# Optimization experiments

Measured on AMD Instinct MI355X. Metric: run time of the kernel, lower is better.

## Reference

```python
import jax, jax.numpy as jnp
import numpy as np

D_MODEL = 1024
N_HEADS = 16
D_K = D_MODEL // N_HEADS
B, S = 4, 2048


def setup_inputs() -> dict:
    key = jax.random.key(0)
    ks = jax.random.split(key, 5)
    scale = 1.0 / np.sqrt(D_MODEL)  # ~xavier scale for square matrices
    return {
        "Q": jax.random.normal(ks[0], (B, S, D_MODEL), dtype=jnp.float32),
        "length": jax.random.randint(ks[1], (B,), 1, S, dtype=jnp.int32),
        "Wq": jax.random.normal(ks[2], (D_MODEL, D_MODEL), dtype=jnp.float32) * scale,
        "bq": jnp.zeros((D_MODEL,), dtype=jnp.float32),
        "Wk": jax.random.normal(ks[3], (D_MODEL, D_MODEL), dtype=jnp.float32) * scale,
        "bk": jnp.zeros((D_MODEL,), dtype=jnp.float32),
        "Wv": jax.random.normal(ks[4], (D_MODEL, D_MODEL), dtype=jnp.float32) * scale,
        "bv": jnp.zeros((D_MODEL,), dtype=jnp.float32),
    }


def reference(Q, length, Wq, bq, Wk, bk, Wv, bv):
    b, s, d = Q.shape
    q_a = Q @ Wq + bq                                   # [b, s, d]
    # split heads: [b, h, s, d_k]
    q_s = q_a.reshape(b, s, N_HEADS, D_K).transpose(0, 2, 1, 3)
    k_s = (Q @ Wk + bk).reshape(b, s, N_HEADS, D_K).transpose(0, 2, 1, 3)
    v_s = (Q @ Wv + bv).reshape(b, s, N_HEADS, D_K).transpose(0, 2, 1, 3)

    # unnormalized exp attention with multiplicative key mask (faithful to source)
    scores = jnp.einsum("bhqd,bhkd->bhqk", q_s, k_s) / np.sqrt(D_K)
    scores = jnp.exp(scores)
    key_mask = (jnp.arange(s)[None, :] < length[:, None]).astype(scores.dtype)  # [b, k]
    scores = scores * key_mask[:, None, None, :]        # broadcast over heads, queries
    attn = scores / (jnp.sum(scores, axis=-1, keepdims=True) + 1e-8)
    context = jnp.einsum("bhqk,bhkd->bhqd", attn, v_s)
    context = context.transpose(0, 2, 1, 3).reshape(b, s, d)
    return context, q_a
```

## Files before the change

kernel.cpp:

```cpp
#include <hip/hip_runtime.h>

#define D_MODEL 1024
#define N_HEADS 16
#define D_KH    64
#define BATCH   4
#define SEQ     2048
#define M_TOTAL (BATCH*SEQ)

typedef __attribute__((ext_vector_type(8))) short short8;
typedef __attribute__((ext_vector_type(4))) float f32x4;
typedef __attribute__((ext_vector_type(4))) unsigned short u16x4;
typedef __attribute__((ext_vector_type(2))) unsigned int u32x2;

__device__ __forceinline__ unsigned short f2bf(float f) {
  union { float f; unsigned u; } v; v.f = f;
  unsigned r = v.u + 0x7FFFu + ((v.u >> 16) & 1u);
  return (unsigned short)(r >> 16);
}
__device__ __forceinline__ unsigned fbits(float f) {
  union { float f; unsigned u; } v; v.f = f; return v.u;
}

__global__ __launch_bounds__(256) void cvt_all(
    const float* __restrict__ Q, unsigned short* __restrict__ Qbf,
    const float* __restrict__ Wq, const float* __restrict__ Wk,
    const float* __restrict__ Wv, unsigned short* __restrict__ WT) {
  __shared__ float tile[32][33];
  const int bid = blockIdx.x;
  if (bid < 8192) {
    size_t i = (size_t)bid * 256 + threadIdx.x;
    float4 v = ((const float4*)Q)[i];
    u16x4 o;
    o[0] = f2bf(v.x); o[1] = f2bf(v.y); o[2] = f2bf(v.z); o[3] = f2bf(v.w);
    ((u16x4*)Qbf)[i] = o;
  } else {
    const int r = bid - 8192;
    const int z = r >> 10;
    const int rem = r & 1023;
    const int k0 = (rem >> 5) * 32, n0 = (rem & 31) * 32;
    const float* W = (z == 0) ? Wq : (z == 1) ? Wk : Wv;
    const int tx = threadIdx.x & 31, ty = threadIdx.x >> 5;
    for (int i = 0; i < 4; ++i)
      tile[ty + i * 8][tx] = W[(size_t)(k0 + ty + i * 8) * D_MODEL + n0 + tx];
    __syncthreads();
    unsigned short* out = WT + (size_t)z * D_MODEL * D_MODEL;
    for (int i = 0; i < 4; ++i)
      out[(size_t)(n0 + ty + i * 8) * D_MODEL + k0 + tx] = f2bf(tile[tx][ty + i * 8]);
  }
}

#define GQ_BM 128
#define GQ_BN 128
#define GQ_BK 64
#define GQ_NT (D_MODEL / GQ_BK)

__global__ __launch_bounds__(256, 2) void gemm_qkv(
    const unsigned short* __restrict__ Qbf,
    const unsigned short* __restrict__ WT,
    const float* __restrict__ bq_p, const float* __restrict__ bk_p,
    const float* __restrict__ bv_p,
    float* __restrict__ out_qa,
    unsigned short* __restrict__ kbf,
    unsigned short* __restrict__ vt) {
  const int f   = blockIdx.x;
  const int swz = (f & 7) * 192 + (f >> 3);
  const int mm  = swz / 24;
  const int nn  = swz % 24;
  const int m0  = mm * GQ_BM;
  const int n0g = nn * GQ_BN;
  const int z   = n0g >> 10;
  const int n0  = n0g & 1023;

  __shared__ unsigned short smA[2][GQ_BM * GQ_BK];
  __shared__ unsigned short smB[2][GQ_BN * GQ_BK];

  const int t    = threadIdx.x;
  const int lane = t & 63;
  const int w    = t >> 6;
  const int quad = lane >> 4;
  const int l16  = lane & 15;
  const int wr   = w >> 1, wc = w & 1;

  f32x4 acc[4][4];
  for (int i = 0; i < 4; ++i)
    for (int j = 0; j < 4; ++j) acc[i][j] = (f32x4){0.f, 0.f, 0.f, 0.f};

  auto stage = [&](int p, int kt) {
    #pragma unroll
    for (int r = 0; r < 4; ++r) {
      int o   = (r * 256 + t) * 8;
      int row = o >> 6;
      int col = (o & 63) ^ ((row & 7) << 3);
      const unsigned short* ga = Qbf + (size_t)(m0 + row)  * D_MODEL + kt * 64 + col;
      const unsigned short* gb = WT  + (size_t)(n0g + row) * D_MODEL + kt * 64 + col;
      __builtin_amdgcn_global_load_lds(
          (const __attribute__((address_space(1))) void*)ga,
          (__attribute__((address_space(3))) void*)&smA[p][o], 16, 0, 0);
      __builtin_amdgcn_global_load_lds(
          (const __attribute__((address_space(1))) void*)gb,
          (__attribute__((address_space(3))) void*)&smB[p][o], 16, 0, 0);
    }
  };

  stage(0, 0);
  stage(1, 1);
  asm volatile("s_waitcnt vmcnt(8)" ::: "memory");
  __builtin_amdgcn_s_barrier();
  asm volatile("" ::: "memory");

  for (int kt = 0; kt < GQ_NT; ++kt) {
    const int p = kt & 1;

    short8 af[4][2], bf[4][2];
    #pragma unroll
    for (int mi = 0; mi < 4; ++mi) {
      int row = wr * 64 + mi * 16 + l16;
      #pragma unroll
      for (int kk = 0; kk < 2; ++kk)
        af[mi][kk] = *(const short8*)
            &smA[p][(row * 64 + kk * 32 + quad * 8) ^ ((row & 7) << 3)];
    }
    #pragma unroll
    for (int ni = 0; ni < 4; ++ni) {
      int row = wc * 64 + ni * 16 + l16;
      #pragma unroll
      for (int kk = 0; kk < 2; ++kk)
        bf[ni][kk] = *(const short8*)
            &smB[p][(row * 64 + kk * 32 + quad * 8) ^ ((row & 7) << 3)];
    }

    __builtin_amdgcn_s_setprio(1);
    #pragma unroll
    for (int mi = 0; mi < 4; ++mi)
      #pragma unroll
      for (int ni = 0; ni < 4; ++ni) {
        acc[mi][ni] = __builtin_amdgcn_mfma_f32_16x16x32_bf16(
            af[mi][0], bf[ni][0], acc[mi][ni], 0, 0, 0);
        acc[mi][ni] = __builtin_amdgcn_mfma_f32_16x16x32_bf16(
            af[mi][1], bf[ni][1], acc[mi][ni], 0, 0, 0);
      }
    __builtin_amdgcn_s_setprio(0);

    __builtin_amdgcn_s_barrier();
    asm volatile("" ::: "memory");
    if (kt + 2 < GQ_NT) {
      stage(p, kt + 2);
      asm volatile("s_waitcnt vmcnt(8)" ::: "memory");
    } else {
      asm volatile("s_waitcnt vmcnt(0)" ::: "memory");
    }
    __builtin_amdgcn_s_barrier();
    asm volatile("" ::: "memory");
  }

  const float* bias = (z == 0) ? bq_p : (z == 1) ? bk_p : bv_p;
  if (z == 2) {
    for (int ni = 0; ni < 4; ++ni) {
      int n = n0 + wc * 64 + ni * 16 + l16;
      float bval = bias[n];
      int h = n >> 6, d = n & 63;
      for (int mi = 0; mi < 4; ++mi) {
        int m = m0 + wr * 64 + mi * 16 + quad * 4;
        int b = m >> 11, s = m & 2047;
        u16x4 o;
        for (int j = 0; j < 4; ++j) o[j] = f2bf(acc[mi][ni][j] + bval);
        *(u16x4*)&vt[(size_t)((b * 16 + h) * 64 + d) * SEQ + s] = o;
      }
    }
  } else {
    for (int ni = 0; ni < 4; ++ni) {
      int n = n0 + wc * 64 + ni * 16 + l16;
      float bval = bias[n];
      for (int mi = 0; mi < 4; ++mi) {
        int mbase = m0 + wr * 64 + mi * 16 + quad * 4;
        for (int j = 0; j < 4; ++j) {
          float v = acc[mi][ni][j] + bval;
          size_t idx = (size_t)(mbase + j) * D_MODEL + n;
          if (z == 0) out_qa[idx] = v;
          else        kbf[idx] = f2bf(v);
        }
      }
    }
  }
}

#define PST 72
#define QBLK 128

__global__ __launch_bounds__(256, 4) void attn(
    const float* __restrict__ qa,
    const unsigned short* __restrict__ kbf,
    const unsigned short* __restrict__ vt,
    const int* __restrict__ length,
    float* __restrict__ ctx) {
  const int flat = blockIdx.y * 16 + blockIdx.x;
  const int low = flat & 3;
  const int mid = (flat >> 2) & 15;
  const int hi  = flat >> 6;
  const int b  = (low + mid + (mid >> 2) + hi + (hi >> 2)) & 3;
  const int h  = mid;
  const int qt = hi;
  const int bh = b * 16 + h;
  const int len = length[b];

  const int t    = threadIdx.x;
  const int lane = t & 63;
  const int w    = t >> 6;
  const int quad = lane >> 4;
  const int l16  = lane & 15;
  const int r8   = t >> 3;
  const int c8   = (t & 7) * 8;

  __shared__ unsigned short sQ[QBLK * PST];
  __shared__ unsigned short sK[64 * PST];
  __shared__ unsigned short sVT[64 * PST];
  unsigned short* const sP = sQ;

  const float SCL = 0.125f * 1.44269504f;

  for (int half = 0; half < 4; ++half) {
    int r = r8 + half * 32;
    const float* src = qa + (size_t)(b * SEQ + qt * QBLK + r) * D_MODEL + h * D_KH + c8;
    float4 v0 = *(const float4*)src;
    float4 v1 = *(const float4*)(src + 4);
    short8 o;
    o[0] = (short)f2bf(v0.x * SCL); o[1] = (short)f2bf(v0.y * SCL);
    o[2] = (short)f2bf(v0.z * SCL); o[3] = (short)f2bf(v0.w * SCL);
    o[4] = (short)f2bf(v1.x * SCL); o[5] = (short)f2bf(v1.y * SCL);
    o[6] = (short)f2bf(v1.z * SCL); o[7] = (short)f2bf(v1.w * SCL);
    *(short8*)&sQ[r * PST + c8] = o;
  }
  __syncthreads();

  const int qr0 = w * 16 + l16;
  const int qr1 = 64 + qr0;
  short8 qf00 = *(const short8*)&sQ[qr0 * PST + quad * 8];
  short8 qf01 = *(const short8*)&sQ[qr0 * PST + 32 + quad * 8];
  short8 qf10 = *(const short8*)&sQ[qr1 * PST + quad * 8];
  short8 qf11 = *(const short8*)&sQ[qr1 * PST + 32 + quad * 8];

  f32x4 acc0[4], acc1[4];
  for (int i = 0; i < 4; ++i) {
    acc0[i] = (f32x4){0.f, 0.f, 0.f, 0.f};
    acc1[i] = (f32x4){0.f, 0.f, 0.f, 0.f};
  }
  float den0 = 0.f, den1 = 0.f;

  const unsigned short* kbase_p = kbf + (size_t)b * SEQ * D_MODEL + h * D_KH;
  const unsigned short* vbase_p = vt + (size_t)bh * 64 * SEQ;

  const int nkt = (len + 63) >> 6;

  short8 rk[2], rv[2];
  for (int half = 0; half < 2; ++half) {
    int r = r8 + half * 32;
    rk[half] = *(const short8*)(kbase_p + (size_t)r * D_MODEL + c8);
    rv[half] = *(const short8*)(vbase_p + (size_t)r * SEQ + c8);
  }

  for (int kt = 0; kt < nkt; ++kt) {
    __syncthreads();
    for (int half = 0; half < 2; ++half) {
      int r = r8 + half * 32;
      *(short8*)&sK[r * PST + c8]  = rk[half];
      *(short8*)&sVT[r * PST + c8] = rv[half];
    }
    __syncthreads();

    if (kt + 1 < nkt) {
      for (int half = 0; half < 2; ++half) {
        int r = r8 + half * 32;
        rk[half] = *(const short8*)(kbase_p + (size_t)((kt + 1) * 64 + r) * D_MODEL + c8);
        rv[half] = *(const short8*)(vbase_p + (size_t)r * SEQ + (kt + 1) * 64 + c8);
      }
    }

    const bool full = ((kt + 1) << 6) <= len;

    for (int n = 0; n < 4; ++n) {
      short8 kf0 = *(const short8*)&sK[(n * 16 + l16) * PST + quad * 8];
      short8 kf1 = *(const short8*)&sK[(n * 16 + l16) * PST + 32 + quad * 8];
      f32x4 s0 = (f32x4){0.f, 0.f, 0.f, 0.f};
      s0 = __builtin_amdgcn_mfma_f32_16x16x32_bf16(kf0, qf00, s0, 0, 0, 0);
      s0 = __builtin_amdgcn_mfma_f32_16x16x32_bf16(kf1, qf01, s0, 0, 0, 0);
      f32x4 s1 = (f32x4){0.f, 0.f, 0.f, 0.f};
      s1 = __builtin_amdgcn_mfma_f32_16x16x32_bf16(kf0, qf10, s1, 0, 0, 0);
      s1 = __builtin_amdgcn_mfma_f32_16x16x32_bf16(kf1, qf11, s1, 0, 0, 0);

      float e0, e1, e2, e3, f0, f1, f2, f3;
      if (full) {
        e0 = exp2f(s0[0]); e1 = exp2f(s0[1]); e2 = exp2f(s0[2]); e3 = exp2f(s0[3]);
        f0 = exp2f(s1[0]); f1 = exp2f(s1[1]); f2 = exp2f(s1[2]); f3 = exp2f(s1[3]);
      } else {
        int kb = kt * 64 + n * 16 + quad * 4;
        e0 = (kb + 0 < len) ? exp2f(s0[0]) : 0.f;
        e1 = (kb + 1 < len) ? exp2f(s0[1]) : 0.f;
        e2 = (kb + 2 < len) ? exp2f(s0[2]) : 0.f;
        e3 = (kb + 3 < len) ? exp2f(s0[3]) : 0.f;
        f0 = (kb + 0 < len) ? exp2f(s1[0]) : 0.f;
        f1 = (kb + 1 < len) ? exp2f(s1[1]) : 0.f;
        f2 = (kb + 2 < len) ? exp2f(s1[2]) : 0.f;
        f3 = (kb + 3 < len) ? exp2f(s1[3]) : 0.f;
      }
      den0 += (e0 + e1) + (e2 + e3);
      den1 += (f0 + f1) + (f2 + f3);
      u32x2 pk;
      pk[0] = __builtin_amdgcn_perm(fbits(e1), fbits(e0), 0x07060302);
      pk[1] = __builtin_amdgcn_perm(fbits(e3), fbits(e2), 0x07060302);
      *(u32x2*)&sP[qr0 * PST + n * 16 + quad * 4] = pk;
      u32x2 pk1;
      pk1[0] = __builtin_amdgcn_perm(fbits(f1), fbits(f0), 0x07060302);
      pk1[1] = __builtin_amdgcn_perm(fbits(f3), fbits(f2), 0x07060302);
      *(u32x2*)&sP[qr1 * PST + n * 16 + quad * 4] = pk1;
    }

    short8 pf00 = *(const short8*)&sP[qr0 * PST + quad * 8];
    short8 pf01 = *(const short8*)&sP[qr0 * PST + 32 + quad * 8];
    short8 pf10 = *(const short8*)&sP[qr1 * PST + quad * 8];
    short8 pf11 = *(const short8*)&sP[qr1 * PST + 32 + quad * 8];
    for (int n2 = 0; n2 < 4; ++n2) {
      short8 vf0 = *(const short8*)&sVT[(n2 * 16 + l16) * PST + quad * 8];
      short8 vf1 = *(const short8*)&sVT[(n2 * 16 + l16) * PST + 32 + quad * 8];
      acc0[n2] = __builtin_amdgcn_mfma_f32_16x16x32_bf16(vf0, pf00, acc0[n2], 0, 0, 0);
      acc0[n2] = __builtin_amdgcn_mfma_f32_16x16x32_bf16(vf1, pf01, acc0[n2], 0, 0, 0);
      acc1[n2] = __builtin_amdgcn_mfma_f32_16x16x32_bf16(vf0, pf10, acc1[n2], 0, 0, 0);
      acc1[n2] = __builtin_amdgcn_mfma_f32_16x16x32_bf16(vf1, pf11, acc1[n2], 0, 0, 0);
    }
  }

  den0 += __shfl_xor(den0, 16, 64);
  den0 += __shfl_xor(den0, 32, 64);
  den1 += __shfl_xor(den1, 16, 64);
  den1 += __shfl_xor(den1, 32, 64);
  float inv0 = 1.f / (den0 + 1e-8f);
  float inv1 = 1.f / (den1 + 1e-8f);

  {
    int q0 = qt * QBLK + w * 16 + l16;
    float* dst0 = ctx + (size_t)(b * SEQ + q0) * D_MODEL + h * D_KH;
    float* dst1 = dst0 + (size_t)64 * D_MODEL;
    for (int n2 = 0; n2 < 4; ++n2) {
      f32x4 o0 = acc0[n2];
      f32x4 o1 = acc1[n2];
      *(float4*)(dst0 + n2 * 16 + quad * 4) =
          make_float4(o0[0] * inv0, o0[1] * inv0, o0[2] * inv0, o0[3] * inv0);
      *(float4*)(dst1 + n2 * 16 + quad * 4) =
          make_float4(o1[0] * inv1, o1[1] * inv1, o1[2] * inv1, o1[3] * inv1);
    }
  }
}

extern "C" void kernel_launch(void* const* d_in, const int* in_sizes, int n_in,
                              void* d_out, int out_size, void* d_ws, size_t ws_size,
                              hipStream_t stream) {
  const float* Q      = (const float*)d_in[0];
  const int*   length = (const int*)d_in[1];
  const float* Wq     = (const float*)d_in[2];
  const float* bq     = (const float*)d_in[3];
  const float* Wk     = (const float*)d_in[4];
  const float* bk     = (const float*)d_in[5];
  const float* Wv     = (const float*)d_in[6];
  const float* bv     = (const float*)d_in[7];

  float* out_ctx = (float*)d_out;
  float* out_qa  = out_ctx + (size_t)M_TOTAL * D_MODEL;

  char* ws = (char*)d_ws;
  unsigned short* Qbf = (unsigned short*)ws;
  unsigned short* WT  = (unsigned short*)(ws + (size_t)16 * 1024 * 1024);
  unsigned short* Kbf = (unsigned short*)(ws + (size_t)22 * 1024 * 1024);
  unsigned short* Vt  = (unsigned short*)(ws + (size_t)38 * 1024 * 1024);

  hipLaunchKernelGGL(cvt_all, dim3(8192 + 3072), dim3(256), 0, stream,
                     Q, Qbf, Wq, Wk, Wv, WT);
  hipLaunchKernelGGL(gemm_qkv, dim3(64 * 24), dim3(256), 0, stream,
                     Qbf, WT, bq, bk, bv, out_qa, Kbf, Vt);
  hipLaunchKernelGGL(attn, dim3(SEQ / QBLK, BATCH * N_HEADS), dim3(256), 0, stream,
                     out_qa, Kbf, Vt, length, out_ctx);
}
```

Before: 241.4 us.

## Restructure QKV GEMM into 256x256 tiles with 8-wave phased half-tile pipeline

The QKV projection GEMM moves from 128x128 tiles with 4 waves to 256x256 tiles with 8 waves (512 threads), cutting the grid from 1536 to 384 blocks. Each K-tile is split into A/B halves, and loads of the next half-tiles are interleaved with the MFMA work on the current quadrants in eight phases per two K-steps, each phase with its own fine-grained vmcnt wait and barriers. The aim is more data reuse per LDS byte and better overlap of global-to-LDS traffic with compute. The cost is 128 KB of LDS per block, higher register pressure from 32 accumulators, and a small grid of 384 blocks that may leave the 256 CUs poorly balanced.

```diff
diff --git a/kernel.cpp b/kernel.cpp
--- a/kernel.cpp
+++ b/kernel.cpp
@@ -19,6 +19,9 @@
 }
 __device__ __forceinline__ unsigned fbits(float f) {
   union { float f; unsigned u; } v; v.f = f; return v.u;
+}
+__device__ __forceinline__ int sw(int row, int col) {
+  return row * 64 + (col ^ ((row & 7) << 3));
 }
 
 __global__ __launch_bounds__(256) void cvt_all(
@@ -49,12 +52,66 @@
   }
 }
 
-#define GQ_BM 128
-#define GQ_BN 128
-#define GQ_BK 64
-#define GQ_NT (D_MODEL / GQ_BK)
-
-__global__ __launch_bounds__(256, 2) void gemm_qkv(
+#define GQ_NT 16
+
+#define GQ_STAGE_HALF(buf, tile, isB, half) do {                               \
+    int kt_ = (tile) & 15;                                                     \
+    _Pragma("unroll")                                                          \
+    for (int r_ = 0; r_ < 2; ++r_) {                                           \
+      int o_   = (r_ * 512 + t) * 8;                \
+      int row_ = (half) * 128 + (o_ >> 6);                                     \
+      int col_ = (o_ & 63) ^ ((row_ & 7) << 3);       \
+      const unsigned short* g_ = (isB)                                         \
+          ? WT  + (size_t)(n0g + row_) * D_MODEL + kt_ * 64 + col_             \
+          : Qbf + (size_t)(m0  + row_) * D_MODEL + kt_ * 64 + col_;            \
+      unsigned short* l_ = ((isB) ? &smB[buf][0] : &smA[buf][0])               \
+                           + (half) * 8192 + o_;              \
+      __builtin_amdgcn_global_load_lds(                                        \
+          (const __attribute__((address_space(1))) void*)g_,                   \
+          (__attribute__((address_space(3))) void*)l_, 16, 0, 0);              \
+    }                                                                          \
+  } while (0)
+
+#define GQ_PHASE(buf, ah, bh, WAIT4, stTile, stB, stHalf) do {                 \
+    short8 a_[2][4], b_[2][2];                                                 \
+    _Pragma("unroll")                                                          \
+    for (int kh_ = 0; kh_ < 2; ++kh_) {                                        \
+      _Pragma("unroll")                                                        \
+      for (int mi_ = 0; mi_ < 4; ++mi_) {                                      \
+        int row_ = (ah) * 128 + wr * 64 + mi_ * 16 + l16;                      \
+        a_[kh_][mi_] = *(const short8*)&smA[buf][sw(row_, kh_ * 32 + quad * 8)]; \
+      }                                                                        \
+      _Pragma("unroll")                                                        \
+      for (int ni_ = 0; ni_ < 2; ++ni_) {                                      \
+        int row_ = (bh) * 128 + wc * 32 + ni_ * 16 + l16;                      \
+        b_[kh_][ni_] = *(const short8*)&smB[buf][sw(row_, kh_ * 32 + quad * 8)]; \
+      }                                                                        \
+    }                                                                          \
+    GQ_STAGE_HALF(((stTile) & 1), stTile, stB, stHalf);                        \
+    __builtin_amdgcn_s_barrier();                                              \
+    asm volatile("" ::: "memory");                                             \
+    __builtin_amdgcn_s_setprio(1);                                             \
+    _Pragma("unroll")                                                          \
+    for (int mi_ = 0; mi_ < 4; ++mi_) {                                        \
+      _Pragma("unroll")                                                        \
+      for (int ni_ = 0; ni_ < 2; ++ni_) {                                      \
+        acc[(ah) * 4 + mi_][(bh) * 2 + ni_] =                                  \
+            __builtin_amdgcn_mfma_f32_16x16x32_bf16(                           \
+                a_[0][mi_], b_[0][ni_], acc[(ah) * 4 + mi_][(bh) * 2 + ni_],   \
+                0, 0, 0);                                                      \
+        acc[(ah) * 4 + mi_][(bh) * 2 + ni_] =                                  \
+            __builtin_amdgcn_mfma_f32_16x16x32_bf16(                           \
+                a_[1][mi_], b_[1][ni_], acc[(ah) * 4 + mi_][(bh) * 2 + ni_],   \
+                0, 0, 0);                                                      \
+      }                                                                        \
+    }                                                                          \
+    __builtin_amdgcn_s_setprio(0);                                             \
+    if (WAIT4) asm volatile("s_waitcnt vmcnt(4)" ::: "memory");                \
+    __builtin_amdgcn_s_barrier();                                              \
+    asm volatile("" ::: "memory");                                             \
+  } while (0)
+
+__global__ __launch_bounds__(512, 2) void gemm_qkv(
     const unsigned short* __restrict__ Qbf,
     const unsigned short* __restrict__ WT,
     const float* __restrict__ bq_p, const float* __restrict__ bk_p,
@@ -63,121 +120,99 @@
     unsigned short* __restrict__ kbf,
     unsigned short* __restrict__ vt) {
   const int f   = blockIdx.x;
-  const int swz = (f & 7) * 192 + (f >> 3);
-  const int mm  = swz / 24;
-  const int nn  = swz % 24;
-  const int m0  = mm * GQ_BM;
-  const int n0g = nn * GQ_BN;
+  const int swz = (f & 7) * 48 + (f >> 3);
+  const int mm  = swz / 12;
+  const int nn  = swz % 12;
+  const int m0  = mm * 256;
+  const int n0g = nn * 256;
   const int z   = n0g >> 10;
   const int n0  = n0g & 1023;
 
-  __shared__ unsigned short smA[2][GQ_BM * GQ_BK];
-  __shared__ unsigned short smB[2][GQ_BN * GQ_BK];
+  __shared__ unsigned short smA[2][256 * 64];
+  __shared__ unsigned short smB[2][256 * 64];
 
   const int t    = threadIdx.x;
   const int lane = t & 63;
   const int w    = t >> 6;
   const int quad = lane >> 4;
   const int l16  = lane & 15;
-  const int wr   = w >> 1, wc = w & 1;
-
-  f32x4 acc[4][4];
-  for (int i = 0; i < 4; ++i)
+  const int wr   = w >> 2;
+  const int wc   = w & 3;
+
+  f32x4 acc[8][4];
+  #pragma unroll
+  for (int i = 0; i < 8; ++i)
+    #pragma unroll
     for (int j = 0; j < 4; ++j) acc[i][j] = (f32x4){0.f, 0.f, 0.f, 0.f};
 
-  auto stage = [&](int p, int kt) {
-    #pragma unroll
-    for (int r = 0; r < 4; ++r) {
-      int o   = (r * 256 + t) * 8;
-      int row = o >> 6;
-      int col = (o & 63) ^ ((row & 7) << 3);
-      const unsigned short* ga = Qbf + (size_t)(m0 + row)  * D_MODEL + kt * 64 + col;
-      const unsigned short* gb = WT  + (size_t)(n0g + row) * D_MODEL + kt * 64 + col;
-      __builtin_amdgcn_global_load_lds(
-          (const __attribute__((address_space(1))) void*)ga,
-          (__attribute__((address_space(3))) void*)&smA[p][o], 16, 0, 0);
-      __builtin_amdgcn_global_load_lds(
-          (const __attribute__((address_space(1))) void*)gb,
-          (__attribute__((address_space(3))) void*)&smB[p][o], 16, 0, 0);
-    }
-  };
-
-  stage(0, 0);
-  stage(1, 1);
-  asm volatile("s_waitcnt vmcnt(8)" ::: "memory");
+  GQ_STAGE_HALF(0, 0, 0, 0);
+  GQ_STAGE_HALF(0, 0, 1, 1);
+  GQ_STAGE_HALF(0, 0, 1, 0);
+  GQ_STAGE_HALF(0, 0, 0, 1);
+  GQ_STAGE_HALF(1, 1, 0, 0);
+  GQ_STAGE_HALF(1, 1, 1, 1);
+  asm volatile("s_waitcnt vmcnt(4)" ::: "memory");
   __builtin_amdgcn_s_barrier();
   asm volatile("" ::: "memory");
 
-  for (int kt = 0; kt < GQ_NT; ++kt) {
-    const int p = kt & 1;
-
-    short8 af[4][2], bf[4][2];
-    #pragma unroll
-    for (int mi = 0; mi < 4; ++mi) {
-      int row = wr * 64 + mi * 16 + l16;
-      #pragma unroll
-      for (int kk = 0; kk < 2; ++kk)
-        af[mi][kk] = *(const short8*)
-            &smA[p][(row * 64 + kk * 32 + quad * 8) ^ ((row & 7) << 3)];
-    }
-    #pragma unroll
-    for (int ni = 0; ni < 4; ++ni) {
-      int row = wc * 64 + ni * 16 + l16;
-      #pragma unroll
-      for (int kk = 0; kk < 2; ++kk)
-        bf[ni][kk] = *(const short8*)
-            &smB[p][(row * 64 + kk * 32 + quad * 8) ^ ((row & 7) << 3)];
-    }
-
-    __builtin_amdgcn_s_setprio(1);
-    #pragma unroll
-    for (int mi = 0; mi < 4; ++mi)
-      #pragma unroll
-      for (int ni = 0; ni < 4; ++ni) {
-        acc[mi][ni] = __builtin_amdgcn_mfma_f32_16x16x32_bf16(
-            af[mi][0], bf[ni][0], acc[mi][ni], 0, 0, 0);
-        acc[mi][ni] = __builtin_amdgcn_mfma_f32_16x16x32_bf16(
-            af[mi][1], bf[ni][1], acc[mi][ni], 0, 0, 0);
-      }
-    __builtin_amdgcn_s_setprio(0);
-
-    __builtin_amdgcn_s_barrier();
-    asm volatile("" ::: "memory");
-    if (kt + 2 < GQ_NT) {
-      stage(p, kt + 2);
-      asm volatile("s_waitcnt vmcnt(8)" ::: "memory");
-    } else {
-      asm volatile("s_waitcnt vmcnt(0)" ::: "memory");
-    }
-    __builtin_amdgcn_s_barrier();
-    asm volatile("" ::: "memory");
-  }
+  for (int i = 0; i < GQ_NT / 2; ++i) {
+    const int e = 2 * i;
+    const int o = 2 * i + 1;
+    GQ_PHASE(0,  0, 0, 0,  o,        1,  0);
+    GQ_PHASE(0,  0, 1, 0,  o,        0,  1);
+    GQ_PHASE(0,  1, 1, 0,  e + 2,    0,  0);
+    GQ_PHASE(0,  1, 0, 1,  e + 2,    1,  1);
+    GQ_PHASE(1,  0, 0, 0,  e + 2,    1,  0);
+    GQ_PHASE(1,  0, 1, 0,  e + 2,    0,  1);
+    GQ_PHASE(1,  1, 1, 0,  o + 2,    0,  0);
+    GQ_PHASE(1,  1, 0, 1,  o + 2,    1,  1);
+  }
+  asm volatile("s_waitcnt vmcnt(0)" ::: "memory");
 
   const float* bias = (z == 0) ? bq_p : (z == 1) ? bk_p : bv_p;
   if (z == 2) {
-    for (int ni = 0; ni < 4; ++ni) {
-      int n = n0 + wc * 64 + ni * 16 + l16;
-      float bval = bias[n];
-      int h = n >> 6, d = n & 63;
-      for (int mi = 0; mi < 4; ++mi) {
-        int m = m0 + wr * 64 + mi * 16 + quad * 4;
-        int b = m >> 11, s = m & 2047;
-        u16x4 o;
-        for (int j = 0; j < 4; ++j) o[j] = f2bf(acc[mi][ni][j] + bval);
-        *(u16x4*)&vt[(size_t)((b * 16 + h) * 64 + d) * SEQ + s] = o;
+    #pragma unroll
+    for (int bh = 0; bh < 2; ++bh) {
+      #pragma unroll
+      for (int ni = 0; ni < 2; ++ni) {
+        int n = n0 + bh * 128 + wc * 32 + ni * 16 + l16;
+        float bval = bias[n];
+        int h = n >> 6, d = n & 63;
+        #pragma unroll
+        for (int ah = 0; ah < 2; ++ah) {
+          #pragma unroll
+          for (int mi = 0; mi < 4; ++mi) {
+            int m = m0 + ah * 128 + wr * 64 + mi * 16 + quad * 4;
+            int b = m >> 11, s = m & 2047;
+            u16x4 oo;
+            #pragma unroll
+            for (int j = 0; j < 4; ++j)
+              oo[j] = f2bf(acc[ah * 4 + mi][bh * 2 + ni][j] + bval);
+            *(u16x4*)&vt[(size_t)((b * 16 + h) * 64 + d) * SEQ + s] = oo;
+          }
+        }
       }
     }
   } else {
-    for (int ni = 0; ni < 4; ++ni) {
-      int n = n0 + wc * 64 + ni * 16 + l16;
-      float bval = bias[n];
-      for (int mi = 0; mi < 4; ++mi) {
-        int mbase = m0 + wr * 64 + mi * 16 + quad * 4;
-        for (int j = 0; j < 4; ++j) {
-          float v = acc[mi][ni][j] + bval;
-          size_t idx = (size_t)(mbase + j) * D_MODEL + n;
-          if (z == 0) out_qa[idx] = v;
-          else        kbf[idx] = f2bf(v);
+    #pragma unroll
+    for (int bh = 0; bh < 2; ++bh) {
+      #pragma unroll
+      for (int ni = 0; ni < 2; ++ni) {
+        int n = n0 + bh * 128 + wc * 32 + ni * 16 + l16;
+        float bval = bias[n];
+        #pragma unroll
+        for (int ah = 0; ah < 2; ++ah) {
+          #pragma unroll
+          for (int mi = 0; mi < 4; ++mi) {
+            int mbase = m0 + ah * 128 + wr * 64 + mi * 16 + quad * 4;
+            #pragma unroll
+            for (int j = 0; j < 4; ++j) {
+              float v = acc[ah * 4 + mi][bh * 2 + ni][j] + bval;
+              size_t idx = (size_t)(mbase + j) * D_MODEL + n;
+              if (z == 0) out_qa[idx] = v;
+              else        kbf[idx] = f2bf(v);
+            }
+          }
         }
       }
     }
@@ -373,7 +408,7 @@
 
   hipLaunchKernelGGL(cvt_all, dim3(8192 + 3072), dim3(256), 0, stream,
                      Q, Qbf, Wq, Wk, Wv, WT);
-  hipLaunchKernelGGL(gemm_qkv, dim3(64 * 24), dim3(256), 0, stream,
+  hipLaunchKernelGGL(gemm_qkv, dim3(384), dim3(512), 0, stream,
                      Qbf, WT, bq, bk, bv, out_qa, Kbf, Vt);
   hipLaunchKernelGGL(attn, dim3(SEQ / QBLK, BATCH * N_HEADS), dim3(256), 0, stream,
                      out_qa, Kbf, Vt, length, out_ctx);
```

Result: slower. 272.6 us (+12.9%).
